# Kernel tuning notes

Hardware: AMD Instinct MI355X
Metric: run time of the kernel (lower is better)

## Reference

```python
import jax, jax.numpy as jnp
import numpy as np
from jax.scipy.special import gammaln

# sizes (see shape_source)
N_CELLS = 1024
N_GENES = 1000
N_LATENT = 50
NB_ENC = 16          # encoder histogram bins per gene
NB_DEC = 16          # decoder mixture components (sum(n_decoder_bins))
N_HID = 16           # encoder hidden dim
N_CUTS = 4_000_000
N_FRAGS = 2_000_000
N_TOTAL_CELLS = 10_000
N_TOTAL_CUTS = 50_000_000
BN_EPS = 1e-5


def _normal_logprob(x, loc, scale):
    z = (x - loc) / scale
    return -0.5 * z * z - jnp.log(scale) - 0.5 * jnp.log(2.0 * jnp.pi)


def setup_inputs() -> dict:
    key = jax.random.key(0)
    ks = jax.random.split(key, 20)
    cut_coordinates = jax.random.uniform(ks[0], (N_CUTS,), dtype=jnp.float32)
    cut_cell = jax.random.randint(ks[1], (N_CUTS,), 0, N_CELLS)
    cut_local_gene_ix = jax.random.randint(ks[2], (N_CUTS,), 0, N_GENES)
    cut_local_cellxgene_ix = cut_cell * N_GENES + cut_local_gene_ix
    local_cellxgene_ix = jax.random.randint(ks[3], (N_FRAGS,), 0, N_CELLS * N_GENES)
    genes_oi = jnp.arange(N_GENES)
    cells_oi = jnp.arange(N_CELLS)
    eps = jax.random.normal(ks[4], (N_CELLS, N_LATENT), dtype=jnp.float32)
    n_in = N_GENES * NB_ENC
    enc_W1 = jax.random.normal(ks[5], (n_in, N_HID)) * (1.0 / np.sqrt(n_in))
    enc_b1 = jnp.zeros((N_HID,))
    bn_gamma = jnp.ones((N_HID,))
    bn_beta = jnp.zeros((N_HID,))
    W_loc = jax.random.normal(ks[6], (N_HID, N_LATENT)) * (1.0 / np.sqrt(N_HID))
    b_loc = jnp.zeros((N_LATENT,))
    W_scale = jax.random.normal(ks[7], (N_HID, N_LATENT)) * (1.0 / np.sqrt(N_HID))
    b_scale = jnp.zeros((N_LATENT,))
    logit_weight = jax.random.normal(ks[8], (N_GENES, N_LATENT, NB_DEC)) * 0.05
    rho_weight = jax.random.normal(ks[9], (N_GENES, N_LATENT)) * 0.05
    baseline_heights = jax.random.normal(ks[10], (N_GENES, NB_DEC)) * 0.1
    libsize = jax.random.randint(ks[11], (N_TOTAL_CELLS,), 1000, 20000)
    rho_bias = jax.random.uniform(ks[12], (N_GENES,), minval=1e-4, maxval=1e-2)
    return dict(
        cut_coordinates=cut_coordinates, eps=eps,
        enc_W1=enc_W1, enc_b1=enc_b1, bn_gamma=bn_gamma, bn_beta=bn_beta,
        W_loc=W_loc, b_loc=b_loc, W_scale=W_scale, b_scale=b_scale,
        logit_weight=logit_weight, rho_weight=rho_weight,
        baseline_heights=baseline_heights, rho_bias=rho_bias,
        cut_local_cellxgene_ix=cut_local_cellxgene_ix,
        cut_local_gene_ix=cut_local_gene_ix,
        local_cellxgene_ix=local_cellxgene_ix,
        genes_oi=genes_oi, cells_oi=cells_oi, libsize=libsize,
    )


def reference(cut_coordinates, eps, enc_W1, enc_b1, bn_gamma, bn_beta,
              W_loc, b_loc, W_scale, b_scale, logit_weight, rho_weight,
              baseline_heights, rho_bias, cut_local_cellxgene_ix,
              cut_local_gene_ix, local_cellxgene_ix, genes_oi, cells_oi,
              libsize):
    n_cells = cells_oi.shape[0]
    n_genes = genes_oi.shape[0]

    # ---- Encoder: digitize + bincount histogram ----
    bin_enc = jnp.minimum(jnp.floor(cut_coordinates * NB_ENC), NB_ENC - 1).astype(jnp.int32)
    digitized = bin_enc + cut_local_cellxgene_ix.astype(jnp.int32) * NB_ENC
    counts = jax.ops.segment_sum(jnp.ones_like(cut_coordinates), digitized,
                                 num_segments=n_cells * n_genes * NB_ENC)
    x = jnp.log1p(counts.reshape(n_cells, n_genes * NB_ENC))  # [C, G*NB]

    h = x @ enc_W1 + enc_b1
    mu = h.mean(axis=0)
    var = h.var(axis=0)  # biased, matches torch BN in train mode
    h = (h - mu) / jnp.sqrt(var + BN_EPS) * bn_gamma + bn_beta
    h = jax.nn.relu(h)
    loc = h @ W_loc + b_loc                 # [C, L]
    scale = jnp.exp(h @ W_scale + b_scale)  # [C, L]

    # ---- latent sample + KL ----
    q_scale = scale * 0.1
    latent = loc + q_scale * eps
    latent_kl = (_normal_logprob(latent, 0.0, 1.0)
                 - _normal_logprob(latent, loc, q_scale)) * (N_TOTAL_CELLS / n_cells)

    # ---- Decoder (n_layers=0: per-gene linear heads) ----
    lw = logit_weight[genes_oi]                       # [G, L, K]
    rw = rho_weight[genes_oi]                         # [G, L]
    mixture_delta = jnp.einsum('cl,glk->cgk', latent, lw)  # [C, G, K]
    rho_delta = jnp.einsum('cl,gl->cg', latent, rw)        # [C, G]
    md_cxg = mixture_delta.reshape(n_cells * n_genes, NB_DEC)
    md_cut = md_cxg[cut_local_cellxgene_ix]           # [N_CUTS, K] gather
    mixture_delta_kl = _normal_logprob(lw, 0.0, 0.1)

    # ---- mixture likelihood: piecewise-constant spline density per cut ----
    logits = baseline_heights[cut_local_gene_ix] + md_cut  # [N_CUTS, K]
    logp = jax.nn.log_softmax(logits, axis=-1)
    bin_dec = jnp.minimum(jnp.floor(cut_coordinates * NB_DEC), NB_DEC - 1).astype(jnp.int32)
    likelihood_mixture = (jnp.take_along_axis(logp, bin_dec[:, None], axis=1)[:, 0]
                          + jnp.log(float(NB_DEC)))

    # ---- fragment-count Poisson likelihood ----
    fragexpr = (rho_bias[genes_oi][None, :] * jnp.exp(rho_delta)
                * libsize[cells_oi].astype(jnp.float32)[:, None])  # [C, G]
    fragmentcounts = jax.ops.segment_sum(
        jnp.ones((local_cellxgene_ix.shape[0],), jnp.float32),
        local_cellxgene_ix, num_segments=n_cells * n_genes
    ).reshape(n_cells, n_genes)
    likelihood_frag = (fragmentcounts * jnp.log(fragexpr) - fragexpr
                       - gammaln(fragmentcounts + 1.0))

    rho_delta_kl = _normal_logprob(rw, 0.0, 0.1)

    likelihood = (likelihood_mixture.sum() * (N_TOTAL_CUTS / cut_coordinates.shape[0])
                  + likelihood_frag.sum() * (N_TOTAL_CELLS / n_cells))
    elbo = (-likelihood - latent_kl.sum() - mixture_delta_kl.sum()
            - rho_delta_kl.sum())
    return elbo
```

## Files before the change

kernel.cpp:

```cpp
#include <hip/hip_runtime.h>
#include <hip/hip_bf16.h>
#include <math.h>


#define G_      1000
#define C_      1024
#define L_      50
#define K_      16
#define NHID_   16
#define CUT_SCALE   12.5f
#define CELL_SCALE  9.765625f

#define CHUNK_    6144
#define RCAP_CUT  18432
#define RCAP_FRAG 9216

#define GCNTC_OFF  0ull
#define GCNTF_OFF  1024ull
#define DONE_OFF   2048ull
#define DACC_OFF   6400ull
#define HT_OFF     6912ull
#define ZERO_BYTES 72448ull
#define LATBF_OFF  72448ull
#define LWT_OFF    203520ull
#define ENTC_OFF   2251520ull
#define ENTF_OFF   11688704ull
#define MERGED_OFF 16407296ull
#define FRAGU8_OFF 24599296ull
#define LATT_OFF   25623296ull
#define WS_NEED    25828096ull

typedef __attribute__((ext_vector_type(8))) short short8;
typedef __attribute__((ext_vector_type(4))) float f32x4;

__device__ __constant__ float LGT[32] = {
    0.0f, 0.0f, 0.6931471805599453f, 1.791759469228055f, 3.1780538303479458f,
    4.787491742782046f, 6.579251212010101f, 8.525161361065415f,
    10.60460290274525f, 12.801827480081469f, 15.104412573075516f,
    17.502307845873887f, 19.987214495661885f, 22.552163853123425f,
    25.19122118273868f, 27.89927138384089f, 30.671860106080672f,
    33.50507345013689f, 36.39544520803305f, 39.339884187199495f,
    42.335616460753485f, 45.38013889847691f, 48.47118135183523f,
    51.60667556776438f, 54.78472939811232f, 58.00360522298052f,
    61.261701761002f, 64.55753862700633f, 67.88974313718154f,
    71.25703896716801f, 74.65823634883016f, 78.0922235533153f };

__device__ __forceinline__ double atomAddF64(double* p, double v) {
    return __hip_atomic_fetch_add(p, v, __ATOMIC_RELAXED,
                                  __HIP_MEMORY_SCOPE_AGENT);
}

__device__ __forceinline__ float block_sum_256(float v) {
    __shared__ float sm[256];
    int t = threadIdx.x;
    __syncthreads();
    sm[t] = v;
    __syncthreads();
#pragma unroll
    for (int s = 128; s > 0; s >>= 1) {
        if (t < s) sm[t] += sm[t + s];
        __syncthreads();
    }
    return sm[0];
}

__global__ __launch_bounds__(256)
void part_kernel(const int* __restrict__ cut_ix,
                 const float* __restrict__ coord,
                 const int* __restrict__ frag_ix,
                 unsigned int* __restrict__ gcnt_c,
                 unsigned int* __restrict__ gcnt_f,
                 unsigned short* __restrict__ entc,
                 unsigned short* __restrict__ entf,
                 const float* __restrict__ lw,
                 const float* __restrict__ rw,
                 __hip_bfloat16* __restrict__ lwT,
                 double* __restrict__ dacc,
                 int n_cuts, int n_frags, int ncc, int nblk_part) {
    int t = threadIdx.x;
    int bid = blockIdx.x;
    if (bid >= nblk_part) {
        int r = bid - nblk_part;
        if (r < 256) {
            for (int g = r; g < G_; g += 256) {
                for (int i = t; i < L_ * K_; i += 256) {
                    float v = lw[(size_t)g * (L_ * K_) + i];
                    lwT[(size_t)g * 1024 + (i & 15) * 64 + (i >> 4)] =
                        __float2bfloat16(v);
                }
                for (int i = t; i < 16 * 14; i += 256) {
                    int n = i / 14, l = 50 + (i % 14);
                    lwT[(size_t)g * 1024 + n * 64 + l] = __float2bfloat16(0.f);
                }
            }
        } else {
            const int NTOT = G_ * L_ * K_ + G_ * L_;
            int wb = r - 256;
            float s = 0.f;
            for (int i = wb * 256 + t; i < NTOT; i += 256 * 256) {
                float w = (i < G_ * L_ * K_) ? lw[i] : rw[i - G_ * L_ * K_];
                s += fmaf(-50.f * w, w, 1.3836465597893733f);
            }
            s = block_sum_256(s);
            if (t == 0) atomAddF64(&dacc[wb & 63], (double)(-s));
        }
        return;
    }
    __shared__ unsigned int cnt[256], excl[256], cur[256], gbas[256];
    __shared__ unsigned short stage[CHUNK_];
    __shared__ unsigned char bkof[CHUNK_];
    bool isCut = (bid < ncc);
    int blk = isCut ? bid : bid - ncc;
    const int* idx = isCut ? cut_ix : frag_ix;
    int n = isCut ? n_cuts : n_frags;
    int rcap = isCut ? RCAP_CUT : RCAP_FRAG;
    unsigned int* gcount = isCut ? gcnt_c : gcnt_f;
    unsigned short* ent = isCut ? entc : entf;
    int i0 = blk * CHUNK_;
    cnt[t] = 0;
    int4 I[6]; float4 X[6];
    unsigned int vm;
    bool full = (i0 + CHUNK_ <= n);
    if (full) {
        const int4* ip = (const int4*)(idx + i0);
#pragma unroll
        for (int k = 0; k < 6; ++k) I[k] = ip[k * 256 + t];
        if (isCut) {
            const float4* xp = (const float4*)(coord + i0);
#pragma unroll
            for (int k = 0; k < 6; ++k) X[k] = xp[k * 256 + t];
        }
        vm = 0xFFFFFFu;
    } else {
        vm = 0;
#pragma unroll
        for (int k = 0; k < 6; ++k) {
            int r0 = i0 + (k * 256 + t) * 4;
            int* Ii = (int*)&I[k]; float* Xi = (float*)&X[k];
#pragma unroll
            for (int u = 0; u < 4; ++u) {
                bool v = (r0 + u) < n;
                if (v) vm |= 1u << (k * 4 + u);
                Ii[u] = v ? idx[r0 + u] : 0;
                Xi[u] = (v && isCut) ? coord[r0 + u] : 0.f;
            }
        }
    }
    __syncthreads();
#pragma unroll
    for (int k = 0; k < 6; ++k) {
        const int* Ii = (const int*)&I[k];
        const float* Xi = (const float*)&X[k];
#pragma unroll
        for (int u = 0; u < 4; ++u) {
            if (vm & (1u << (k * 4 + u))) {
                int ix = Ii[u];
                int c = ix / G_;
                int g = ix - c * G_;
                unsigned int bk;
                if (isCut) {
                    int b = (int)(Xi[u] * 16.f); b = b > 15 ? 15 : b;
                    bk = ((unsigned)(c >> 6) << 4) | ((unsigned)(g * K_ + b) >> 10);
                } else {
                    bk = ((unsigned)(c >> 6) << 4) | ((unsigned)g >> 6);
                }
                atomicAdd(&cnt[bk], 1u);
            }
        }
    }
    __syncthreads();
    if (t < 64) {
        unsigned int c0 = cnt[t * 4 + 0], c1 = cnt[t * 4 + 1];
        unsigned int c2 = cnt[t * 4 + 2], c3 = cnt[t * 4 + 3];
        unsigned int tot = c0 + c1 + c2 + c3;
        unsigned int run = tot;
#pragma unroll
        for (int o = 1; o < 64; o <<= 1) {
            unsigned int v = __shfl_up(run, o, 64);
            if (t >= o) run += v;
        }
        unsigned int base = run - tot;
        excl[t * 4 + 0] = base;
        excl[t * 4 + 1] = base + c0;
        excl[t * 4 + 2] = base + c0 + c1;
        excl[t * 4 + 3] = base + c0 + c1 + c2;
    }
    __syncthreads();
    gbas[t] = cnt[t] ? atomicAdd(&gcount[t], cnt[t]) : 0u;
    cur[t] = excl[t];
    __syncthreads();
#pragma unroll
    for (int k = 0; k < 6; ++k) {
        const int* Ii = (const int*)&I[k];
        const float* Xi = (const float*)&X[k];
#pragma unroll
        for (int u = 0; u < 4; ++u) {
            if (vm & (1u << (k * 4 + u))) {
                int ix = Ii[u];
                int c = ix / G_;
                int g = ix - c * G_;
                unsigned int bk; unsigned short e;
                if (isCut) {
                    int b = (int)(Xi[u] * 16.f); b = b > 15 ? 15 : b;
                    int bin = g * K_ + b;
                    bk = ((unsigned)(c >> 6) << 4) | ((unsigned)bin >> 10);
                    e = (unsigned short)(((c & 63) << 10) | (bin & 1023));
                } else {
                    bk = ((unsigned)(c >> 6) << 4) | ((unsigned)g >> 6);
                    e = (unsigned short)(((c & 63) << 6) | (g & 63));
                }
                unsigned int p = atomicAdd(&cur[bk], 1u);
                stage[p] = e;
                bkof[p] = (unsigned char)bk;
            }
        }
    }
    __syncthreads();
    int total = n - i0; if (total > CHUNK_) total = CHUNK_;
    for (int p = t; p < total; p += 256) {
        unsigned int bk = bkof[p];
        unsigned int dst = gbas[bk] + (p - excl[bk]);
        if (dst < (unsigned)rcap)
            ent[(size_t)bk * rcap + dst] = stage[p];
    }
}

__global__ __launch_bounds__(256)
void mid_kernel(const unsigned int* __restrict__ gcnt_c,
                const unsigned short* __restrict__ entc,
                const unsigned int* __restrict__ gcnt_f,
                const unsigned short* __restrict__ entf,
                const float* __restrict__ W1,
                unsigned int* __restrict__ merged,
                unsigned int* __restrict__ fragw,
                float* __restrict__ hT) {
    __shared__ unsigned int h[4096];
    __shared__ float w1s[4096];
    int t = threadIdx.x;
    int bid = blockIdx.x;
    if (bid < 1024) {
        int bk = bid >> 2, q = bid & 3;
        int cg = bk >> 4, bc = bk & 15;
        int wbase = (bc * 1024 + q * 256) * NHID_;
#pragma unroll
        for (int r = 0; r < 16; ++r) {
            int i = r * 256 + t;
            int gi = wbase + i;
            w1s[i] = (gi < 16000 * NHID_) ? W1[gi] : 0.f;
        }
        for (int i = t; i < 2048; i += 256) h[i] = 0;
        __syncthreads();
        unsigned int count = gcnt_c[bk];
        if (count > RCAP_CUT) count = RCAP_CUT;
        const unsigned int* e32 = (const unsigned int*)(entc + (size_t)bk * RCAP_CUT);
        unsigned int npair = count >> 1;
        for (unsigned int base = 0; base < npair; base += 1024) {
            unsigned int w[4]; bool val[4];
#pragma unroll
            for (int u = 0; u < 4; ++u) {
                unsigned int p = base + u * 256 + t;
                val[u] = (p < npair);
                w[u] = val[u] ? e32[p] : 0u;
            }
#pragma unroll
            for (int u = 0; u < 4; ++u) {
                if (val[u]) {
                    unsigned int v0 = w[u] & 0xffffu, v1 = w[u] >> 16;
                    unsigned int b0 = v0 & 1023u, b1 = v1 & 1023u;
                    if ((int)(b0 >> 8) == q) {
                        unsigned int c0 = v0 >> 10;
                        atomicAdd(&h[(b0 & 255u) * 8 + (c0 >> 3)],
                                  1u << ((c0 & 7) * 4));
                    }
                    if ((int)(b1 >> 8) == q) {
                        unsigned int c1 = v1 >> 10;
                        atomicAdd(&h[(b1 & 255u) * 8 + (c1 >> 3)],
                                  1u << ((c1 & 7) * 4));
                    }
                }
            }
        }
        if (t == 0 && (count & 1u)) {
            unsigned int v = ((const unsigned short*)e32)[count - 1];
            unsigned int b0 = v & 1023u;
            if ((int)(b0 >> 8) == q) {
                unsigned int c0 = v >> 10;
                atomicAdd(&h[(b0 & 255u) * 8 + (c0 >> 3)], 1u << ((c0 & 7) * 4));
            }
        }
        __syncthreads();
        for (int i = t; i < 2048; i += 256) {
            int bin = bc * 1024 + q * 256 + (i >> 3);
            if (bin < 16000)
                merged[(unsigned)bin * 128u + (unsigned)cg * 8u + (i & 7)] = h[i];
        }
        int c_lo = t & 63, sub = t >> 6;
        float acc[NHID_];
#pragma unroll
        for (int j = 0; j < NHID_; ++j) acc[j] = 0.f;
        int rbase = bc * 1024 + q * 256 + sub * 64;
        int sh = (c_lo & 7) * 4;
        const float4* w1v = (const float4*)w1s;
#pragma unroll 2
        for (int bl = 0; bl < 64; ++bl) {
            int row = rbase + bl;
            if (row < 16000) {
                int rl = sub * 64 + bl;
                unsigned int w = h[rl * 8 + (c_lo >> 3)];
                float xv = __logf((float)(((w >> sh) & 0xfu) + 1u));
                float4 wa = w1v[rl * 4 + 0];
                float4 wb = w1v[rl * 4 + 1];
                float4 wc = w1v[rl * 4 + 2];
                float4 wd = w1v[rl * 4 + 3];
                acc[0] = fmaf(xv, wa.x, acc[0]);  acc[1] = fmaf(xv, wa.y, acc[1]);
                acc[2] = fmaf(xv, wa.z, acc[2]);  acc[3] = fmaf(xv, wa.w, acc[3]);
                acc[4] = fmaf(xv, wb.x, acc[4]);  acc[5] = fmaf(xv, wb.y, acc[5]);
                acc[6] = fmaf(xv, wb.z, acc[6]);  acc[7] = fmaf(xv, wb.w, acc[7]);
                acc[8] = fmaf(xv, wc.x, acc[8]);  acc[9] = fmaf(xv, wc.y, acc[9]);
                acc[10] = fmaf(xv, wc.z, acc[10]); acc[11] = fmaf(xv, wc.w, acc[11]);
                acc[12] = fmaf(xv, wd.x, acc[12]); acc[13] = fmaf(xv, wd.y, acc[13]);
                acc[14] = fmaf(xv, wd.z, acc[14]); acc[15] = fmaf(xv, wd.w, acc[15]);
            }
        }
        __syncthreads();
        float* sp = (float*)h;
#pragma unroll
        for (int j = 0; j < NHID_; ++j) sp[sub * 1024 + j * 64 + c_lo] = acc[j];
        __syncthreads();
        for (int i = t; i < 1024; i += 256) {
            int j = i >> 6, c = i & 63;
            float v = sp[j * 64 + c] + sp[1024 + j * 64 + c]
                    + sp[2048 + j * 64 + c] + sp[3072 + j * 64 + c];
            atomicAdd(&hT[j * C_ + cg * 64 + c], v);
        }
    } else {
        int bk = bid - 1024, cg = bk >> 4, gc = bk & 15;
        for (int i = t; i < 2048; i += 256) h[i] = 0;
        __syncthreads();
        unsigned int count = gcnt_f[bk];
        if (count > RCAP_FRAG) count = RCAP_FRAG;
        const unsigned short* e = entf + (size_t)bk * RCAP_FRAG;
#pragma unroll 4
        for (unsigned int p = t; p < count; p += 256) {
            unsigned int v = e[p];
            unsigned int g_lo = v & 63u;
            unsigned int c_lo = v >> 6;
            atomicAdd(&h[g_lo * 32 + (c_lo >> 1)], 1u << ((c_lo & 1) * 16));
        }
        __syncthreads();
        for (int i = t; i < 1024; i += 256) {
            int g_lo = i >> 4, wb = i & 15;
            unsigned int lo = h[g_lo * 32 + wb * 2];
            unsigned int hi = h[g_lo * 32 + wb * 2 + 1];
            unsigned int outv = (lo & 0xffu) | (((lo >> 16) & 0xffu) << 8)
                              | ((hi & 0xffu) << 16) | (((hi >> 16) & 0xffu) << 24);
            int g = gc * 64 + g_lo;
            if (g < G_)
                fragw[(unsigned)g * 256u + (unsigned)cg * 16u + wb] = outv;
        }
    }
}

__global__ __launch_bounds__(256)
void latent_kernel(const float* __restrict__ hT,
                   const float* __restrict__ gamma,
                   const float* __restrict__ beta,
                   const float* __restrict__ W_loc,
                   const float* __restrict__ b_loc,
                   const float* __restrict__ W_scale,
                   const float* __restrict__ b_scale,
                   const float* __restrict__ eps,
                   float* __restrict__ latT,
                   __hip_bfloat16* __restrict__ latbf,
                   double* __restrict__ dacc) {
    __shared__ float scs[NHID_], shs[NHID_];
    int t = threadIdx.x;
    {
        int j = t >> 4, cl = t & 15;
        double s1 = 0.0, s2 = 0.0;
#pragma unroll 8
        for (int k = 0; k < 64; ++k) {
            float v = hT[j * C_ + cl + k * 16];
            s1 += (double)v; s2 += (double)v * (double)v;
        }
#pragma unroll
        for (int m = 1; m < 16; m <<= 1) {
            s1 += __shfl_xor(s1, m);
            s2 += __shfl_xor(s2, m);
        }
        if (cl == 0) {
            double mean = s1 * (1.0 / C_);
            double var = s2 * (1.0 / C_) - mean * mean;
            float rstd = rsqrtf((float)var + 1e-5f);
            float sc = gamma[j] * rstd;
            scs[j] = sc;
            shs[j] = beta[j] - (float)mean * sc;
        }
    }
    __syncthreads();
    int idx = blockIdx.x * 256 + t;
    float kl = 0.f;
    {
        int c = idx / L_;
        int l = idx - c * L_;
        float hb[NHID_];
#pragma unroll
        for (int j = 0; j < NHID_; ++j) {
            float v = fmaf(hT[j * C_ + c], scs[j], shs[j]);
            hb[j] = v > 0.f ? v : 0.f;
        }
        float loc = b_loc[l], ls = b_scale[l];
#pragma unroll
        for (int j = 0; j < NHID_; ++j) {
            loc = fmaf(hb[j], W_loc[j * L_ + l], loc);
            ls  = fmaf(hb[j], W_scale[j * L_ + l], ls);
        }
        float qs = 0.1f * __expf(ls);
        float e = eps[idx];
        float lat = fmaf(qs, e, loc);
        latT[(size_t)l * C_ + c] = lat;
        latbf[c * 64 + l] = __float2bfloat16(lat);
        if (l < 14) latbf[c * 64 + 50 + l] = __float2bfloat16(0.f);
        float z = (lat - loc) / qs;
        kl = fmaf(-0.5f * lat, lat, fmaf(0.5f * z, z, __logf(qs)));
    }
    float s = block_sum_256(kl);
    if (threadIdx.x == 0)
        atomAddF64(&dacc[blockIdx.x & 63], (double)(-CELL_SCALE * s));
}

__global__ __launch_bounds__(256)
void mixpois_kernel(const __hip_bfloat16* __restrict__ latbf,
                    const __hip_bfloat16* __restrict__ lwT,
                    const unsigned int* __restrict__ merged,
                    const float* __restrict__ baseline,
                    const float* __restrict__ latT,
                    const float* __restrict__ rw,
                    const float* __restrict__ rho_bias,
                    const int* __restrict__ libsize,
                    const unsigned char* __restrict__ fragb,
                    double* __restrict__ dacc,
                    unsigned int* __restrict__ done,
                    float* __restrict__ out) {
    int g = blockIdx.x;
    int y = blockIdx.y;
    int t = threadIdx.x;
    int lane = t & 63;
    int wv = t >> 6;
    int s16 = lane & 15;
    int quad = lane >> 4;
    const __hip_bfloat16* bb = lwT + (size_t)g * 1024 + s16 * 64 + quad * 8;
    short8 lw1 = *(const short8*)bb;
    short8 lw2 = *(const short8*)(bb + 32);
    const float4 bl4 = *(const float4*)(baseline + g * K_ + quad * 4);
    const unsigned int* mrow =
        merged + (size_t)(g * K_ + quad * 4) * 128u;
    float partial = 0.f;
    int cwave = y * 256 + wv * 64;
#pragma unroll
    for (int mt = 0; mt < 4; ++mt) {
        int c0 = cwave + mt * 16;
        const __hip_bfloat16* aa = latbf + (size_t)(c0 + s16) * 64 + quad * 8;
        short8 la1 = *(const short8*)aa;
        short8 la2 = *(const short8*)(aa + 32);
        f32x4 d = {bl4.x, bl4.y, bl4.z, bl4.w};
        d = __builtin_amdgcn_mfma_f32_16x16x32_bf16(lw1, la1, d, 0, 0, 0);
        d = __builtin_amdgcn_mfma_f32_16x16x32_bf16(lw2, la2, d, 0, 0, 0);
        float m = fmaxf(fmaxf(d[0], d[1]), fmaxf(d[2], d[3]));
        m = fmaxf(m, __shfl_xor(m, 16));
        m = fmaxf(m, __shfl_xor(m, 32));
        float e0 = __expf(d[0] - m), e1 = __expf(d[1] - m);
        float e2 = __expf(d[2] - m), e3 = __expf(d[3] - m);
        float S = (e0 + e1) + (e2 + e3);
        S += __shfl_xor(S, 16);
        S += __shfl_xor(S, 32);
        float lse = m + __logf(S);
        int cp = c0 + s16;
        unsigned int widx = (unsigned)cp >> 3;
        int sb = (cp & 7) * 4;
#pragma unroll
        for (int r = 0; r < 4; ++r) {
            float cnt = (float)((mrow[r * 128u + widx] >> sb) & 0xfu);
            partial = fmaf(cnt, d[r] - lse, partial);
        }
    }
    float v;
    {
        int c = y * 256 + t;
        const float* rwg = rw + (size_t)g * L_;
        float rho = 0.f;
#pragma unroll 10
        for (int l = 0; l < L_; ++l)
            rho = fmaf(latT[l * C_ + c], rwg[l], rho);
        unsigned int fc = fragb[(size_t)g * C_ + c];
        float fe = rho_bias[g] * __expf(rho) * (float)libsize[c];
        float lf = fmaf((float)fc, __logf(fe), -fe) - LGT[fc > 31u ? 31u : fc];
        v = fmaf(-CUT_SCALE, partial, -CELL_SCALE * lf);
    }
    float contrib = block_sum_256(v);
    __shared__ int lastflag;
    if (threadIdx.x == 0) {
        lastflag = 0;
        int slot = blockIdx.x & 63;
        double oldv = atomAddF64(&dacc[slot], (double)contrib);
        unsigned inc = 1u;
        float dep = (float)oldv;
        asm volatile("" : "+v"(inc) : "v"(dep));
        unsigned quota = ((slot < 40) ? 16u : 15u) * 4u;
        if (atomicAdd(&done[slot * 16], inc) == quota - 1u) {
            if (atomicAdd(&done[1024], 1u) == 63u) lastflag = 1;
        }
    }
    __syncthreads();
    if (lastflag) {
        if (t < 64) {
            double dv = atomAddF64(&dacc[t], 0.0);
#pragma unroll
            for (int m = 1; m < 64; m <<= 1) dv += __shfl_xor(dv, m);
            if (t == 0)
                out[0] = (float)(dv - 138629436.11198905);
        }
    }
}

extern "C" void kernel_launch(void* const* d_in, const int* in_sizes, int n_in,
                              void* d_out, int out_size, void* d_ws, size_t ws_size,
                              hipStream_t stream) {
    const float* cut_coord = (const float*)d_in[0];
    const float* eps       = (const float*)d_in[1];
    const float* enc_W1    = (const float*)d_in[2];
    const float* bn_gamma  = (const float*)d_in[4];
    const float* bn_beta   = (const float*)d_in[5];
    const float* W_loc     = (const float*)d_in[6];
    const float* b_loc     = (const float*)d_in[7];
    const float* W_scale   = (const float*)d_in[8];
    const float* b_scale   = (const float*)d_in[9];
    const float* logit_w   = (const float*)d_in[10];
    const float* rho_w     = (const float*)d_in[11];
    const float* baseline  = (const float*)d_in[12];
    const float* rho_bias  = (const float*)d_in[13];
    const int* cut_cxg     = (const int*)d_in[14];
    const int* frag_ix     = (const int*)d_in[16];
    const int* libsize     = (const int*)d_in[19];

    int n_cuts  = in_sizes[0];
    int n_frags = in_sizes[16];

    char* ws = (char*)d_ws;
    unsigned int*   gcnt_c = (unsigned int*)(ws + GCNTC_OFF);
    unsigned int*   gcnt_f = (unsigned int*)(ws + GCNTF_OFF);
    unsigned int*   done   = (unsigned int*)(ws + DONE_OFF);
    double*         dacc   = (double*)(ws + DACC_OFF);
    float*          hT     = (float*)(ws + HT_OFF);
    __hip_bfloat16* latbf  = (__hip_bfloat16*)(ws + LATBF_OFF);
    __hip_bfloat16* lwT    = (__hip_bfloat16*)(ws + LWT_OFF);
    unsigned short* entc   = (unsigned short*)(ws + ENTC_OFF);
    unsigned short* entf   = (unsigned short*)(ws + ENTF_OFF);
    unsigned int*   merged = (unsigned int*)(ws + MERGED_OFF);
    unsigned int*   fragw  = (unsigned int*)(ws + FRAGU8_OFF);
    float*          latT   = (float*)(ws + LATT_OFF);
    float*          out    = (float*)d_out;

    int ncc = (n_cuts + CHUNK_ - 1) / CHUNK_;
    int ncf = (n_frags + CHUNK_ - 1) / CHUNK_;
    int nblk_part = ncc + ncf;

    hipMemsetAsync(ws, 0, ZERO_BYTES, stream);

    part_kernel<<<nblk_part + 512, 256, 0, stream>>>(
        cut_cxg, cut_coord, frag_ix, gcnt_c, gcnt_f, entc, entf,
        logit_w, rho_w, lwT, dacc,
        n_cuts, n_frags, ncc, nblk_part);
    mid_kernel<<<1280, 256, 0, stream>>>(
        gcnt_c, entc, gcnt_f, entf, enc_W1, merged, fragw, hT);
    latent_kernel<<<(C_ * L_) / 256, 256, 0, stream>>>(
        hT, bn_gamma, bn_beta, W_loc, b_loc, W_scale, b_scale,
        eps, latT, latbf, dacc);
    mixpois_kernel<<<dim3(G_, 4), 256, 0, stream>>>(
        latbf, lwT, merged, baseline, latT, rho_w, rho_bias, libsize,
        (const unsigned char*)fragw, dacc, done, out);
}
```

Before: 230.5 us.

## Split cut buckets four ways so mid-kernel blocks read only their own entries

Cut entries are now bucketed into 1024 buckets (64 cell groups by 64 bin groups) in the scatter kernel, up from 256. Each mid_kernel block previously read a whole 1024-bin bucket and threw away three quarters of the entries; now it reads only entries for its own 256-bin quarter. The scatter kernel now runs a 1024-entry scan over all four wavefronts, encodes the high bucket bits into the 16-bit entry, and issues four times as many global count atomics. Shared memory in mid_kernel shrinks and the reduction scratch reuses the weight buffer.

```diff
diff --git a/kernel.cpp b/kernel.cpp
--- a/kernel.cpp
+++ b/kernel.cpp
@@ -11,24 +11,24 @@
 #define CUT_SCALE   12.5f
 #define CELL_SCALE  9.765625f
 
-#define CHUNK_    6144
-#define RCAP_CUT  18432
-#define RCAP_FRAG 9216
+#define CHUNK_     6144
+#define RCAP_CUTQ  4608
+#define RCAP_FRAG  9216
 
 #define GCNTC_OFF  0ull
-#define GCNTF_OFF  1024ull
-#define DONE_OFF   2048ull
-#define DACC_OFF   6400ull
-#define HT_OFF     6912ull
-#define ZERO_BYTES 72448ull
-#define LATBF_OFF  72448ull
-#define LWT_OFF    203520ull
-#define ENTC_OFF   2251520ull
-#define ENTF_OFF   11688704ull
-#define MERGED_OFF 16407296ull
-#define FRAGU8_OFF 24599296ull
-#define LATT_OFF   25623296ull
-#define WS_NEED    25828096ull
+#define GCNTF_OFF  4096ull
+#define DONE_OFF   5120ull
+#define DACC_OFF   9728ull
+#define HT_OFF     10240ull
+#define ZERO_BYTES 75776ull
+#define LATBF_OFF  75776ull
+#define LWT_OFF    206848ull
+#define ENTC_OFF   2254848ull
+#define ENTF_OFF   11692032ull
+#define MERGED_OFF 16410624ull
+#define FRAGU8_OFF 24602624ull
+#define LATT_OFF   25626624ull
+#define WS_NEED    25831424ull
 
 typedef __attribute__((ext_vector_type(8))) short short8;
 typedef __attribute__((ext_vector_type(4))) float f32x4;
@@ -106,18 +106,19 @@
         }
         return;
     }
-    __shared__ unsigned int cnt[256], excl[256], cur[256], gbas[256];
+    __shared__ unsigned int cnt[1024], cur[1024], gbas[1024];
+    __shared__ unsigned int wtot[4];
     __shared__ unsigned short stage[CHUNK_];
     __shared__ unsigned char bkof[CHUNK_];
     bool isCut = (bid < ncc);
     int blk = isCut ? bid : bid - ncc;
     const int* idx = isCut ? cut_ix : frag_ix;
     int n = isCut ? n_cuts : n_frags;
-    int rcap = isCut ? RCAP_CUT : RCAP_FRAG;
+    unsigned int rcap = isCut ? RCAP_CUTQ : RCAP_FRAG;
     unsigned int* gcount = isCut ? gcnt_c : gcnt_f;
     unsigned short* ent = isCut ? entc : entf;
     int i0 = blk * CHUNK_;
-    cnt[t] = 0;
+    cnt[t] = 0; cnt[t + 256] = 0; cnt[t + 512] = 0; cnt[t + 768] = 0;
     int4 I[6]; float4 X[6];
     unsigned int vm;
     bool full = (i0 + CHUNK_ <= n);
@@ -160,7 +161,7 @@
                 unsigned int bk;
                 if (isCut) {
                     int b = (int)(Xi[u] * 16.f); b = b > 15 ? 15 : b;
-                    bk = ((unsigned)(c >> 6) << 4) | ((unsigned)(g * K_ + b) >> 10);
+                    bk = ((unsigned)(c >> 6) << 6) | ((unsigned)(g * K_ + b) >> 8);
                 } else {
                     bk = ((unsigned)(c >> 6) << 4) | ((unsigned)g >> 6);
                 }
@@ -169,25 +170,32 @@
         }
     }
     __syncthreads();
-    if (t < 64) {
+    {
         unsigned int c0 = cnt[t * 4 + 0], c1 = cnt[t * 4 + 1];
         unsigned int c2 = cnt[t * 4 + 2], c3 = cnt[t * 4 + 3];
         unsigned int tot = c0 + c1 + c2 + c3;
         unsigned int run = tot;
+        int lane = t & 63, wv = t >> 6;
 #pragma unroll
         for (int o = 1; o < 64; o <<= 1) {
             unsigned int v = __shfl_up(run, o, 64);
-            if (t >= o) run += v;
-        }
-        unsigned int base = run - tot;
-        excl[t * 4 + 0] = base;
-        excl[t * 4 + 1] = base + c0;
-        excl[t * 4 + 2] = base + c0 + c1;
-        excl[t * 4 + 3] = base + c0 + c1 + c2;
-    }
-    __syncthreads();
-    gbas[t] = cnt[t] ? atomicAdd(&gcount[t], cnt[t]) : 0u;
-    cur[t] = excl[t];
+            if (lane >= o) run += v;
+        }
+        if (lane == 63) wtot[wv] = run;
+        __syncthreads();
+        unsigned int wb = 0;
+#pragma unroll
+        for (int w = 0; w < 3; ++w) if (w < wv) wb += wtot[w];
+        unsigned int base = wb + run - tot;
+        cur[t * 4 + 0] = base;
+        cur[t * 4 + 1] = base + c0;
+        cur[t * 4 + 2] = base + c0 + c1;
+        cur[t * 4 + 3] = base + c0 + c1 + c2;
+        gbas[t * 4 + 0] = c0 ? atomicAdd(&gcount[t * 4 + 0], c0) : 0u;
+        gbas[t * 4 + 1] = c1 ? atomicAdd(&gcount[t * 4 + 1], c1) : 0u;
+        gbas[t * 4 + 2] = c2 ? atomicAdd(&gcount[t * 4 + 2], c2) : 0u;
+        gbas[t * 4 + 3] = c3 ? atomicAdd(&gcount[t * 4 + 3], c3) : 0u;
+    }
     __syncthreads();
 #pragma unroll
     for (int k = 0; k < 6; ++k) {
@@ -203,8 +211,9 @@
                 if (isCut) {
                     int b = (int)(Xi[u] * 16.f); b = b > 15 ? 15 : b;
                     int bin = g * K_ + b;
-                    bk = ((unsigned)(c >> 6) << 4) | ((unsigned)bin >> 10);
-                    e = (unsigned short)(((c & 63) << 10) | (bin & 1023));
+                    bk = ((unsigned)(c >> 6) << 6) | ((unsigned)bin >> 8);
+                    e = (unsigned short)(((bk >> 8) << 14) |
+                                         ((c & 63) << 8) | (bin & 255));
                 } else {
                     bk = ((unsigned)(c >> 6) << 4) | ((unsigned)g >> 6);
                     e = (unsigned short)(((c & 63) << 6) | (g & 63));
@@ -218,10 +227,12 @@
     __syncthreads();
     int total = n - i0; if (total > CHUNK_) total = CHUNK_;
     for (int p = t; p < total; p += 256) {
-        unsigned int bk = bkof[p];
-        unsigned int dst = gbas[bk] + (p - excl[bk]);
-        if (dst < (unsigned)rcap)
-            ent[(size_t)bk * rcap + dst] = stage[p];
+        unsigned int e = stage[p];
+        unsigned int bk = ((e >> 14) << 8) | bkof[p];
+        unsigned int beg = cur[bk] - cnt[bk];
+        unsigned int dst = gbas[bk] + (p - beg);
+        if (dst < rcap)
+            ent[(size_t)bk * rcap + dst] = (unsigned short)e;
     }
 }
 
@@ -234,14 +245,14 @@
                 unsigned int* __restrict__ merged,
                 unsigned int* __restrict__ fragw,
                 float* __restrict__ hT) {
-    __shared__ unsigned int h[4096];
+    __shared__ unsigned int h[2048];
     __shared__ float w1s[4096];
     int t = threadIdx.x;
     int bid = blockIdx.x;
     if (bid < 1024) {
-        int bk = bid >> 2, q = bid & 3;
-        int cg = bk >> 4, bc = bk & 15;
-        int wbase = (bc * 1024 + q * 256) * NHID_;
+        int bk = bid;
+        int cg = bk >> 6, bgrp = bk & 63;
+        int wbase = (bgrp * 256) * NHID_;
 #pragma unroll
         for (int r = 0; r < 16; ++r) {
             int i = r * 256 + t;
@@ -251,8 +262,8 @@
         for (int i = t; i < 2048; i += 256) h[i] = 0;
         __syncthreads();
         unsigned int count = gcnt_c[bk];
-        if (count > RCAP_CUT) count = RCAP_CUT;
-        const unsigned int* e32 = (const unsigned int*)(entc + (size_t)bk * RCAP_CUT);
+        if (count > RCAP_CUTQ) count = RCAP_CUTQ;
+        const unsigned int* e32 = (const unsigned int*)(entc + (size_t)bk * RCAP_CUTQ);
         unsigned int npair = count >> 1;
         for (unsigned int base = 0; base < npair; base += 1024) {
             unsigned int w[4]; bool val[4];
@@ -266,31 +277,22 @@
             for (int u = 0; u < 4; ++u) {
                 if (val[u]) {
                     unsigned int v0 = w[u] & 0xffffu, v1 = w[u] >> 16;
-                    unsigned int b0 = v0 & 1023u, b1 = v1 & 1023u;
-                    if ((int)(b0 >> 8) == q) {
-                        unsigned int c0 = v0 >> 10;
-                        atomicAdd(&h[(b0 & 255u) * 8 + (c0 >> 3)],
-                                  1u << ((c0 & 7) * 4));
-                    }
-                    if ((int)(b1 >> 8) == q) {
-                        unsigned int c1 = v1 >> 10;
-                        atomicAdd(&h[(b1 & 255u) * 8 + (c1 >> 3)],
-                                  1u << ((c1 & 7) * 4));
-                    }
+                    unsigned int c0 = (v0 >> 8) & 63u, c1 = (v1 >> 8) & 63u;
+                    atomicAdd(&h[(v0 & 255u) * 8 + (c0 >> 3)],
+                              1u << ((c0 & 7) * 4));
+                    atomicAdd(&h[(v1 & 255u) * 8 + (c1 >> 3)],
+                              1u << ((c1 & 7) * 4));
                 }
             }
         }
         if (t == 0 && (count & 1u)) {
             unsigned int v = ((const unsigned short*)e32)[count - 1];
-            unsigned int b0 = v & 1023u;
-            if ((int)(b0 >> 8) == q) {
-                unsigned int c0 = v >> 10;
-                atomicAdd(&h[(b0 & 255u) * 8 + (c0 >> 3)], 1u << ((c0 & 7) * 4));
-            }
+            unsigned int c0 = (v >> 8) & 63u;
+            atomicAdd(&h[(v & 255u) * 8 + (c0 >> 3)], 1u << ((c0 & 7) * 4));
         }
         __syncthreads();
         for (int i = t; i < 2048; i += 256) {
-            int bin = bc * 1024 + q * 256 + (i >> 3);
+            int bin = bgrp * 256 + (i >> 3);
             if (bin < 16000)
                 merged[(unsigned)bin * 128u + (unsigned)cg * 8u + (i & 7)] = h[i];
         }
@@ -298,7 +300,7 @@
         float acc[NHID_];
 #pragma unroll
         for (int j = 0; j < NHID_; ++j) acc[j] = 0.f;
-        int rbase = bc * 1024 + q * 256 + sub * 64;
+        int rbase = bgrp * 256 + sub * 64;
         int sh = (c_lo & 7) * 4;
         const float4* w1v = (const float4*)w1s;
 #pragma unroll 2
@@ -323,7 +325,7 @@
             }
         }
         __syncthreads();
-        float* sp = (float*)h;
+        float* sp = (float*)w1s;
 #pragma unroll
         for (int j = 0; j < NHID_; ++j) sp[sub * 1024 + j * 64 + c_lo] = acc[j];
         __syncthreads();
@@ -344,7 +346,7 @@
         for (unsigned int p = t; p < count; p += 256) {
             unsigned int v = e[p];
             unsigned int g_lo = v & 63u;
-            unsigned int c_lo = v >> 6;
+            unsigned int c_lo = (v >> 6) & 63u;
             atomicAdd(&h[g_lo * 32 + (c_lo >> 1)], 1u << ((c_lo & 1) * 16));
         }
         __syncthreads();
```

Result: slower. 250.1 us (+8.5%).

## Merge four quarter-blocks per bucket into one block with full histogram

Applied to the files above, without the earlier changes.

The cut-histogram part of mid_kernel now uses one block per bucket instead of four. That block holds a 1024-bin histogram in a larger shared array and streams W1 in four 256-row slices. Before, each of the four quarter-blocks read the whole bucket's entries and kept only one quarter of them. The change removes that 4x redundant read and filter, and cuts the hT atomics by 4x. In exchange there are fewer blocks (512 vs 1280), so less parallelism, and more shared memory per block (48KB), which may lower occupancy.

```diff
diff --git a/kernel.cpp b/kernel.cpp
--- a/kernel.cpp
+++ b/kernel.cpp
@@ -234,21 +234,14 @@
                 unsigned int* __restrict__ merged,
                 unsigned int* __restrict__ fragw,
                 float* __restrict__ hT) {
-    __shared__ unsigned int h[4096];
+    __shared__ unsigned int h[8192];
     __shared__ float w1s[4096];
     int t = threadIdx.x;
     int bid = blockIdx.x;
-    if (bid < 1024) {
-        int bk = bid >> 2, q = bid & 3;
+    if (bid < 256) {
+        int bk = bid;
         int cg = bk >> 4, bc = bk & 15;
-        int wbase = (bc * 1024 + q * 256) * NHID_;
-#pragma unroll
-        for (int r = 0; r < 16; ++r) {
-            int i = r * 256 + t;
-            int gi = wbase + i;
-            w1s[i] = (gi < 16000 * NHID_) ? W1[gi] : 0.f;
-        }
-        for (int i = t; i < 2048; i += 256) h[i] = 0;
+        for (int i = t; i < 8192; i += 256) h[i] = 0;
         __syncthreads();
         unsigned int count = gcnt_c[bk];
         if (count > RCAP_CUT) count = RCAP_CUT;
@@ -266,31 +259,22 @@
             for (int u = 0; u < 4; ++u) {
                 if (val[u]) {
                     unsigned int v0 = w[u] & 0xffffu, v1 = w[u] >> 16;
-                    unsigned int b0 = v0 & 1023u, b1 = v1 & 1023u;
-                    if ((int)(b0 >> 8) == q) {
-                        unsigned int c0 = v0 >> 10;
-                        atomicAdd(&h[(b0 & 255u) * 8 + (c0 >> 3)],
-                                  1u << ((c0 & 7) * 4));
-                    }
-                    if ((int)(b1 >> 8) == q) {
-                        unsigned int c1 = v1 >> 10;
-                        atomicAdd(&h[(b1 & 255u) * 8 + (c1 >> 3)],
-                                  1u << ((c1 & 7) * 4));
-                    }
+                    unsigned int c0 = v0 >> 10, c1 = v1 >> 10;
+                    atomicAdd(&h[(v0 & 1023u) * 8 + (c0 >> 3)],
+                              1u << ((c0 & 7) * 4));
+                    atomicAdd(&h[(v1 & 1023u) * 8 + (c1 >> 3)],
+                              1u << ((c1 & 7) * 4));
                 }
             }
         }
         if (t == 0 && (count & 1u)) {
             unsigned int v = ((const unsigned short*)e32)[count - 1];
-            unsigned int b0 = v & 1023u;
-            if ((int)(b0 >> 8) == q) {
-                unsigned int c0 = v >> 10;
-                atomicAdd(&h[(b0 & 255u) * 8 + (c0 >> 3)], 1u << ((c0 & 7) * 4));
-            }
-        }
-        __syncthreads();
-        for (int i = t; i < 2048; i += 256) {
-            int bin = bc * 1024 + q * 256 + (i >> 3);
+            unsigned int c0 = v >> 10;
+            atomicAdd(&h[(v & 1023u) * 8 + (c0 >> 3)], 1u << ((c0 & 7) * 4));
+        }
+        __syncthreads();
+        for (int i = t; i < 8192; i += 256) {
+            int bin = bc * 1024 + (i >> 3);
             if (bin < 16000)
                 merged[(unsigned)bin * 128u + (unsigned)cg * 8u + (i & 7)] = h[i];
         }
@@ -298,32 +282,44 @@
         float acc[NHID_];
 #pragma unroll
         for (int j = 0; j < NHID_; ++j) acc[j] = 0.f;
-        int rbase = bc * 1024 + q * 256 + sub * 64;
         int sh = (c_lo & 7) * 4;
-        const float4* w1v = (const float4*)w1s;
+        for (int qq = 0; qq < 4; ++qq) {
+            __syncthreads();
+            int wbase = (bc * 1024 + qq * 256) * NHID_;
+#pragma unroll
+            for (int r = 0; r < 16; ++r) {
+                int i = r * 256 + t;
+                int gi = wbase + i;
+                w1s[i] = (gi < 16000 * NHID_) ? W1[gi] : 0.f;
+            }
+            __syncthreads();
+            const float4* w1v = (const float4*)w1s;
+            int rl0 = qq * 256 + sub * 64;
 #pragma unroll 2
-        for (int bl = 0; bl < 64; ++bl) {
-            int row = rbase + bl;
-            if (row < 16000) {
-                int rl = sub * 64 + bl;
-                unsigned int w = h[rl * 8 + (c_lo >> 3)];
-                float xv = __logf((float)(((w >> sh) & 0xfu) + 1u));
-                float4 wa = w1v[rl * 4 + 0];
-                float4 wb = w1v[rl * 4 + 1];
-                float4 wc = w1v[rl * 4 + 2];
-                float4 wd = w1v[rl * 4 + 3];
-                acc[0] = fmaf(xv, wa.x, acc[0]);  acc[1] = fmaf(xv, wa.y, acc[1]);
-                acc[2] = fmaf(xv, wa.z, acc[2]);  acc[3] = fmaf(xv, wa.w, acc[3]);
-                acc[4] = fmaf(xv, wb.x, acc[4]);  acc[5] = fmaf(xv, wb.y, acc[5]);
-                acc[6] = fmaf(xv, wb.z, acc[6]);  acc[7] = fmaf(xv, wb.w, acc[7]);
-                acc[8] = fmaf(xv, wc.x, acc[8]);  acc[9] = fmaf(xv, wc.y, acc[9]);
-                acc[10] = fmaf(xv, wc.z, acc[10]); acc[11] = fmaf(xv, wc.w, acc[11]);
-                acc[12] = fmaf(xv, wd.x, acc[12]); acc[13] = fmaf(xv, wd.y, acc[13]);
-                acc[14] = fmaf(xv, wd.z, acc[14]); acc[15] = fmaf(xv, wd.w, acc[15]);
-            }
-        }
-        __syncthreads();
-        float* sp = (float*)h;
+            for (int bl = 0; bl < 64; ++bl) {
+                int row = bc * 1024 + rl0 + bl;
+                if (row < 16000) {
+                    int rh = rl0 + bl;
+                    int rw2 = sub * 64 + bl;
+                    unsigned int w = h[rh * 8 + (c_lo >> 3)];
+                    float xv = __logf((float)(((w >> sh) & 0xfu) + 1u));
+                    float4 wa = w1v[rw2 * 4 + 0];
+                    float4 wb = w1v[rw2 * 4 + 1];
+                    float4 wc = w1v[rw2 * 4 + 2];
+                    float4 wd = w1v[rw2 * 4 + 3];
+                    acc[0] = fmaf(xv, wa.x, acc[0]);  acc[1] = fmaf(xv, wa.y, acc[1]);
+                    acc[2] = fmaf(xv, wa.z, acc[2]);  acc[3] = fmaf(xv, wa.w, acc[3]);
+                    acc[4] = fmaf(xv, wb.x, acc[4]);  acc[5] = fmaf(xv, wb.y, acc[5]);
+                    acc[6] = fmaf(xv, wb.z, acc[6]);  acc[7] = fmaf(xv, wb.w, acc[7]);
+                    acc[8] = fmaf(xv, wc.x, acc[8]);  acc[9] = fmaf(xv, wc.y, acc[9]);
+                    acc[10] = fmaf(xv, wc.z, acc[10]); acc[11] = fmaf(xv, wc.w, acc[11]);
+                    acc[12] = fmaf(xv, wd.x, acc[12]); acc[13] = fmaf(xv, wd.y, acc[13]);
+                    acc[14] = fmaf(xv, wd.z, acc[14]); acc[15] = fmaf(xv, wd.w, acc[15]);
+                }
+            }
+        }
+        __syncthreads();
+        float* sp = (float*)w1s;
 #pragma unroll
         for (int j = 0; j < NHID_; ++j) sp[sub * 1024 + j * 64 + c_lo] = acc[j];
         __syncthreads();
@@ -334,7 +330,7 @@
             atomicAdd(&hT[j * C_ + cg * 64 + c], v);
         }
     } else {
-        int bk = bid - 1024, cg = bk >> 4, gc = bk & 15;
+        int bk = bid - 256, cg = bk >> 4, gc = bk & 15;
         for (int i = t; i < 2048; i += 256) h[i] = 0;
         __syncthreads();
         unsigned int count = gcnt_f[bk];
@@ -344,7 +340,7 @@
         for (unsigned int p = t; p < count; p += 256) {
             unsigned int v = e[p];
             unsigned int g_lo = v & 63u;
-            unsigned int c_lo = v >> 6;
+            unsigned int c_lo = (v >> 6) & 63u;
             atomicAdd(&h[g_lo * 32 + (c_lo >> 1)], 1u << ((c_lo & 1) * 16));
         }
         __syncthreads();
@@ -571,7 +567,7 @@
         cut_cxg, cut_coord, frag_ix, gcnt_c, gcnt_f, entc, entf,
         logit_w, rho_w, lwT, dacc,
         n_cuts, n_frags, ncc, nblk_part);
-    mid_kernel<<<1280, 256, 0, stream>>>(
+    mid_kernel<<<512, 256, 0, stream>>>(
         gcnt_c, entc, gcnt_f, entf, enc_W1, merged, fragw, hT);
     latent_kernel<<<(C_ * L_) / 256, 256, 0, stream>>>(
         hT, bn_gamma, bn_beta, W_loc, b_loc, W_scale, b_scale,
```

Result: slower. 244.5 us (+6.1%).
